# Performance work log

Measured on AMD Instinct MI355X. Metric: run time of the kernel, lower is better.

The kernel has to match this reference:

```python
import jax, jax.numpy as jnp
import numpy as np

# --- constants from loss_param_dict (fallback norm_info: means=0, stds=1 -> denorm is identity) ---
A_DIV, A_NS, A_BC = 0.3, 0.3, 0.3
A_LOSS = 1.0 - A_DIV - A_NS - A_BC
SCALE_BASE, SCALE_DIV, SCALE_NS, SCALE_BC = 300000.0, 1e-05, 0.01, 1.0
SX, SY = 1.2 / 127, 0.8 / 127  # spacing along axis 2 (x) and axis 1 (y)
RHO, MU = 1.0, 1.0
H, W = 128, 128
IN_TOP = H // 2 + H // 16 + 1  # 73
IN_BOT = H // 2 - H // 16 - 1  # 55
NORM_MEAN = np.array([0.0, 0.0, 0.0, 0.0], dtype=np.float32)
NORM_STD = np.array([1.0, 1.0, 1.0, 1.0], dtype=np.float32)


def grad_axis(f, h, axis):
    """torch.gradient: 2nd-order central interior, 1st-order one-sided edges."""
    f = jnp.moveaxis(f, axis, -1)
    left = (f[..., 1:2] - f[..., 0:1]) / h
    interior = (f[..., 2:] - f[..., :-2]) / (2.0 * h)
    right = (f[..., -1:] - f[..., -2:-1]) / h
    g = jnp.concatenate([left, interior, right], axis=-1)
    return jnp.moveaxis(g, -1, axis)


def setup_inputs() -> dict:
    key = jax.random.key(0)
    k1, k2, k3 = jax.random.split(key, 3)
    B = 256
    return {
        "inputs": jax.random.normal(k1, (B, 1, H, W), dtype=jnp.float32),
        "outputs": jax.random.normal(k2, (B, 3, H, W), dtype=jnp.float32),
        "targets": jax.random.normal(k3, (B, 3, H, W), dtype=jnp.float32),
    }


def reference(inputs, outputs, targets):
    # base MSE loss (reduction='sum')
    loss_base = jnp.sum((outputs - targets) ** 2) / SCALE_BASE

    # denormalisation (norm_info fallback: identity, but kept for faithfulness)
    in_ch = inputs.shape[1]
    mean = jnp.asarray(NORM_MEAN)
    std = jnp.asarray(NORM_STD)
    inp = inputs * std[:in_ch][None, :, None, None] + mean[:in_ch][None, :, None, None]
    out = outputs * std[in_ch:][None, :, None, None] + mean[in_ch:][None, :, None, None]

    # boundary residual pieces (on full, un-cropped denormalised outputs)
    pieces = [
        out[:, 1, IN_BOT:IN_TOP, 0].ravel() - 0.01,
        out[:, 0, IN_BOT:IN_TOP, -1].ravel(),
    ]
    for ch in (1, 2):
        for idx in (0, -1):
            pieces += [
                out[:, ch, idx, :].ravel(),
                out[:, ch, IN_TOP:, idx].ravel(),
                out[:, ch, 0:IN_BOT, idx].ravel(),
            ]
    boundary = jnp.concatenate(pieces)

    # interior crop [B, C, 126, 126]
    i_loc = inp[:, :, 1 : H - 1, 1 : W - 1]
    o_loc = out[:, :, 1 : H - 1, 1 : W - 1]

    p, u, v = o_loc[:, 0], o_loc[:, 1], o_loc[:, 2]  # [B,126,126]
    alpha = i_loc[:, 0]

    dp_dx, dp_dy = grad_axis(p, SX, 2), grad_axis(p, SY, 1)
    du_dx, du_dy = grad_axis(u, SX, 2), grad_axis(u, SY, 1)
    dv_dx, dv_dy = grad_axis(v, SX, 2), grad_axis(v, SY, 1)
    du_dxx = grad_axis(du_dx, SX, 2)
    du_dyy = grad_axis(du_dy, SY, 1)
    dv_dxx = grad_axis(dv_dx, SX, 2)
    dv_dyy = grad_axis(dv_dy, SY, 1)

    # continuity residual
    loss_cont = jnp.mean((du_dx + dv_dy) ** 2) / SCALE_DIV

    # Navier-Stokes residual
    x_res = u * du_dx + v * du_dy + dp_dx / RHO - MU * (du_dxx + du_dyy) / RHO + alpha * u / RHO
    y_res = u * dv_dx + v * dv_dy + dp_dy / RHO - MU * (dv_dxx + dv_dyy) / RHO + alpha * v / RHO
    mse_ns = (jnp.mean(x_res**2, axis=(1, 2)) + jnp.mean(y_res**2, axis=(1, 2))).mean() / 2.0
    loss_ns = mse_ns / SCALE_NS

    # boundary residual
    loss_bc = jnp.mean(boundary**2) / SCALE_BC

    return A_LOSS * loss_base + A_DIV * loss_cont + A_NS * loss_ns + A_BC * loss_bc
```

## Files before the change

### kernel.cpp

```cpp
#include <hip/hip_runtime.h>


#define HH 128
#define WW 128
#define NI 126
#define NBLK 4096

#define AS1C(p) ((const __attribute__((address_space(1))) void*)(p))
#define AS3(p)  ((__attribute__((address_space(3))) void*)(p))

template <int I> __device__ __forceinline__ float gc(const float4& f) {
    if constexpr (I == 0) return f.x;
    else if constexpr (I == 1) return f.y;
    else if constexpr (I == 2) return f.z;
    else return f.w;
}

template <int IDX>
__device__ __forceinline__ float xsel(const float4& l, const float4& m, const float4& r) {
    if constexpr (IDX < 4) return gc<IDX>(l);
    else if constexpr (IDX < 8) return gc<IDX - 4>(m);
    else return gc<IDX - 8>(r);
}

__device__ __forceinline__ float grad1s(float m1, float a0, float p1, int i,
                                        float inv_h, float inv_2h) {
    if (i == 0) return (p1 - a0) * inv_h;
    if (i == NI - 1) return (a0 - m1) * inv_h;
    return (p1 - m1) * inv_2h;
}

__device__ __forceinline__ float grad2s(float m2, float m1, float a0, float p1, float p2,
                                        int i, float inv_h, float inv_2h) {
    if (i == 0) {
        const float d1 = (p2 - a0) * inv_2h, d0 = (p1 - a0) * inv_h;
        return (d1 - d0) * inv_h;
    }
    if (i == 1) {
        const float d1 = (p2 - a0) * inv_2h, dm1 = (a0 - m1) * inv_h;
        return (d1 - dm1) * inv_2h;
    }
    if (i == NI - 1) {
        const float d0 = (a0 - m1) * inv_h, dm1 = (a0 - m2) * inv_2h;
        return (d0 - dm1) * inv_h;
    }
    if (i == NI - 2) {
        const float d1 = (p1 - a0) * inv_h, dm1 = (a0 - m2) * inv_2h;
        return (d1 - dm1) * inv_2h;
    }
    return (p2 - 2.f * a0 + m2) * inv_2h * inv_2h;
}

struct Acc { float base, bc, cont, ns; };

template <int Q>
__device__ __forceinline__ void do_pixel(
    int r, int c0, bool midrow,
    const float4& uxl, const float4& uxm, const float4& uxr,
    const float4& uym2, const float4& uym1, const float4& uyp1, const float4& uyp2,
    const float4& vxl, const float4& vxm, const float4& vxr,
    const float4& vym2, const float4& vym1, const float4& vyp1, const float4& vyp2,
    const float4& pxl, const float4& pxm, const float4& pxr,
    const float4& pym1, const float4& pyp1,
    const float4& t0, const float4& t1, const float4& t2, const float4& av,
    Acc& acc) {
    const int c = c0 + Q;
    const float u0 = xsel<Q + 4>(uxl, uxm, uxr);
    const float v0 = xsel<Q + 4>(vxl, vxm, vxr);
    const float p0 = xsel<Q + 4>(pxl, pxm, pxr);

    {
        const float d0 = p0 - gc<Q>(t0);
        const float d1 = u0 - gc<Q>(t1);
        const float d2 = v0 - gc<Q>(t2);
        acc.base += d0 * d0 + d1 * d1 + d2 * d2;
    }
    if (c == 0 && midrow) { const float d = u0 - 0.01f; acc.bc += d * d; }
    if (c == WW - 1 && midrow) { acc.bc += p0 * p0; }
    if (r == 0 || r == HH - 1) { acc.bc += u0 * u0 + v0 * v0; }
    if ((c == 0 || c == WW - 1) && !midrow) { acc.bc += u0 * u0 + v0 * v0; }

    if (r >= 1 && r <= HH - 2 && c >= 1 && c <= WW - 2) {
        const int ic = c - 1, ir = r - 1;
        const float inv_sx = 127.0f / 1.2f, inv_2sx = 127.0f / 2.4f;
        const float inv_sy = 127.0f / 0.8f, inv_2sy = 127.0f / 1.6f;

        const float uxm2 = xsel<Q + 2>(uxl, uxm, uxr), uxm1 = xsel<Q + 3>(uxl, uxm, uxr);
        const float uxp1 = xsel<Q + 5>(uxl, uxm, uxr), uxp2 = xsel<Q + 6>(uxl, uxm, uxr);
        const float vxm2 = xsel<Q + 2>(vxl, vxm, vxr), vxm1 = xsel<Q + 3>(vxl, vxm, vxr);
        const float vxp1 = xsel<Q + 5>(vxl, vxm, vxr), vxp2 = xsel<Q + 6>(vxl, vxm, vxr);
        const float pxm1 = xsel<Q + 3>(pxl, pxm, pxr), pxp1 = xsel<Q + 5>(pxl, pxm, pxr);
        const float uym2s = gc<Q>(uym2), uym1s = gc<Q>(uym1);
        const float uyp1s = gc<Q>(uyp1), uyp2s = gc<Q>(uyp2);
        const float vym2s = gc<Q>(vym2), vym1s = gc<Q>(vym1);
        const float vyp1s = gc<Q>(vyp1), vyp2s = gc<Q>(vyp2);
        const float pym1s = gc<Q>(pym1), pyp1s = gc<Q>(pyp1);

        const float du_dx = grad1s(uxm1, u0, uxp1, ic, inv_sx, inv_2sx);
        const float du_dy = grad1s(uym1s, u0, uyp1s, ir, inv_sy, inv_2sy);
        const float dv_dx = grad1s(vxm1, v0, vxp1, ic, inv_sx, inv_2sx);
        const float dv_dy = grad1s(vym1s, v0, vyp1s, ir, inv_sy, inv_2sy);
        const float dp_dx = grad1s(pxm1, p0, pxp1, ic, inv_sx, inv_2sx);
        const float dp_dy = grad1s(pym1s, p0, pyp1s, ir, inv_sy, inv_2sy);
        const float du_dxx = grad2s(uxm2, uxm1, u0, uxp1, uxp2, ic, inv_sx, inv_2sx);
        const float du_dyy = grad2s(uym2s, uym1s, u0, uyp1s, uyp2s, ir, inv_sy, inv_2sy);
        const float dv_dxx = grad2s(vxm2, vxm1, v0, vxp1, vxp2, ic, inv_sx, inv_2sx);
        const float dv_dyy = grad2s(vym2s, vym1s, v0, vyp1s, vyp2s, ir, inv_sy, inv_2sy);

        const float alpha = gc<Q>(av);
        const float dvg = du_dx + dv_dy;
        acc.cont += dvg * dvg;
        const float xr_ = u0 * du_dx + v0 * du_dy + dp_dx - (du_dxx + du_dyy) + alpha * u0;
        const float yr_ = u0 * dv_dx + v0 * dv_dy + dp_dy - (dv_dxx + dv_dyy) + alpha * v0;
        acc.ns += xr_ * xr_ + yr_ * yr_;
    }
}

__global__ __launch_bounds__(256) void physics_loss_kernel(
    const float* __restrict__ inp, const float* __restrict__ out,
    const float* __restrict__ tgt, double* __restrict__ ws) {
    const int tid = threadIdx.x;
    const int grp = tid & 31;
    const int rloc = tid >> 5;
    const int bid = ((blockIdx.x & 7) << 9) | (blockIdx.x >> 3);
    const int b = bid >> 4;
    const int r0 = (bid & 15) << 3;
    const int r = r0 | rloc;
    const int c0 = grp << 2;
    const int lane = tid & 63;
    const int wv = tid >> 6;

    const float* O = out + (size_t)b * 3 * HH * WW;
    const float* T = tgt + (size_t)b * 3 * HH * WW;
    const float* A = inp + (size_t)b * HH * WW;
    const float* P = O;
    const float* U = O + HH * WW;
    const float* V = O + 2 * HH * WW;

    __shared__ float tile[34][128];

    auto ld = [&](const float* base, int row, int gg) {
        return reinterpret_cast<const float4*>(base + row * WW)[gg];
    };
    const float4 t0 = ld(T, r, grp);
    const float4 t1 = ld(T + HH * WW, r, grp);
    const float4 t2 = ld(T + 2 * HH * WW, r, grp);
    const float4 av = ld(A, r, grp);

    const int lsub = lane >> 5;
    const int lcol = (lane & 31) << 2;
    for (int ci = wv; ci < 17; ci += 4) {
        const float* src;
        int grow;
        if (ci < 6)       { src = U; grow = r0 - 2 + ci * 2 + lsub; }
        else if (ci < 12) { src = V; grow = r0 - 2 + (ci - 6) * 2 + lsub; }
        else              { src = P; grow = r0 - 1 + (ci - 12) * 2 + lsub; }
        grow = grow < 0 ? 0 : (grow > 127 ? 127 : grow);
        const float* gaddr = src + grow * WW + lcol;
        __builtin_amdgcn_global_load_lds(AS1C(gaddr),
                                         AS3((char*)&tile[0][0] + ci * 1024),
                                         16, 0, 0);
    }
    __syncthreads();

    const int gl = grp == 0 ? 0 : grp - 1;
    const int gr = grp == 31 ? 31 : grp + 1;
    auto lrow = [&](int row) { return reinterpret_cast<const float4*>(&tile[row][0]); };
    const float4 uym2 = lrow(rloc)[grp],     uym1 = lrow(rloc + 1)[grp];
    const float4 uxl  = lrow(rloc + 2)[gl],  uxm  = lrow(rloc + 2)[grp];
    const float4 uxr  = lrow(rloc + 2)[gr];
    const float4 uyp1 = lrow(rloc + 3)[grp], uyp2 = lrow(rloc + 4)[grp];
    const float4 vym2 = lrow(12 + rloc)[grp],     vym1 = lrow(12 + rloc + 1)[grp];
    const float4 vxl  = lrow(12 + rloc + 2)[gl],  vxm  = lrow(12 + rloc + 2)[grp];
    const float4 vxr  = lrow(12 + rloc + 2)[gr];
    const float4 vyp1 = lrow(12 + rloc + 3)[grp], vyp2 = lrow(12 + rloc + 4)[grp];
    const float4 pym1 = lrow(24 + rloc)[grp];
    const float4 pxl  = lrow(24 + rloc + 1)[gl],  pxm  = lrow(24 + rloc + 1)[grp];
    const float4 pxr  = lrow(24 + rloc + 1)[gr];
    const float4 pyp1 = lrow(24 + rloc + 2)[grp];

    const bool midrow = (r >= 55 && r < 73);
    Acc acc = {0.f, 0.f, 0.f, 0.f};

    do_pixel<0>(r, c0, midrow, uxl, uxm, uxr, uym2, uym1, uyp1, uyp2,
                vxl, vxm, vxr, vym2, vym1, vyp1, vyp2,
                pxl, pxm, pxr, pym1, pyp1, t0, t1, t2, av, acc);
    do_pixel<1>(r, c0, midrow, uxl, uxm, uxr, uym2, uym1, uyp1, uyp2,
                vxl, vxm, vxr, vym2, vym1, vyp1, vyp2,
                pxl, pxm, pxr, pym1, pyp1, t0, t1, t2, av, acc);
    do_pixel<2>(r, c0, midrow, uxl, uxm, uxr, uym2, uym1, uyp1, uyp2,
                vxl, vxm, vxr, vym2, vym1, vyp1, vyp2,
                pxl, pxm, pxr, pym1, pyp1, t0, t1, t2, av, acc);
    do_pixel<3>(r, c0, midrow, uxl, uxm, uxr, uym2, uym1, uyp1, uyp2,
                vxl, vxm, vxr, vym2, vym1, vyp1, vyp2,
                pxl, pxm, pxr, pym1, pyp1, t0, t1, t2, av, acc);

    float a_base = acc.base, a_bc = acc.bc, a_cont = acc.cont, a_ns = acc.ns;
    #pragma unroll
    for (int off = 32; off > 0; off >>= 1) {
        a_base += __shfl_down(a_base, off);
        a_bc   += __shfl_down(a_bc, off);
        a_cont += __shfl_down(a_cont, off);
        a_ns   += __shfl_down(a_ns, off);
    }
    __shared__ float red[4][4];
    if (lane == 0) {
        red[wv][0] = a_base; red[wv][1] = a_bc;
        red[wv][2] = a_cont; red[wv][3] = a_ns;
    }
    __syncthreads();
    if (tid == 0) {
        double b0 = 0, b1 = 0, b2 = 0, b3 = 0;
        #pragma unroll
        for (int w = 0; w < 4; ++w) {
            b0 += red[w][0]; b1 += red[w][1]; b2 += red[w][2]; b3 += red[w][3];
        }
        double* slot = ws + (size_t)bid * 4;
        slot[0] = b0; slot[1] = b1; slot[2] = b2; slot[3] = b3;
    }
}

__global__ __launch_bounds__(256) void finalize_kernel(const double* __restrict__ ws,
                                                       float* __restrict__ out) {
    const int tid = threadIdx.x;
    double a0 = 0, a1 = 0, a2 = 0, a3 = 0;
    for (int b = tid; b < NBLK; b += 256) {
        const double* p = ws + (size_t)b * 4;
        a0 += p[0]; a1 += p[1]; a2 += p[2]; a3 += p[3];
    }
    #pragma unroll
    for (int off = 32; off > 0; off >>= 1) {
        a0 += __shfl_down(a0, off);
        a1 += __shfl_down(a1, off);
        a2 += __shfl_down(a2, off);
        a3 += __shfl_down(a3, off);
    }
    __shared__ double red[4][4];
    const int wave = tid >> 6, lane = tid & 63;
    if (lane == 0) {
        red[wave][0] = a0; red[wave][1] = a1; red[wave][2] = a2; red[wave][3] = a3;
    }
    __syncthreads();
    if (tid == 0) {
        double b0 = 0, b1 = 0, b2 = 0, b3 = 0;
        #pragma unroll
        for (int w = 0; w < 4; ++w) {
            b0 += red[w][0]; b1 += red[w][1]; b2 += red[w][2]; b3 += red[w][3];
        }
        const double loss_base = b0 / 300000.0;
        const double loss_cont = b2 / (256.0 * 126.0 * 126.0) / 1e-5;
        const double loss_ns   = b3 / (2.0 * 256.0 * 126.0 * 126.0) / 0.01;
        const double loss_bc   = b1 / (256.0 * 988.0);
        out[0] = (float)(0.10000000000000009 * loss_base +
                         0.3 * (loss_cont + loss_ns + loss_bc));
    }
}

extern "C" void kernel_launch(void* const* d_in, const int* in_sizes, int n_in,
                              void* d_out, int out_size, void* d_ws, size_t ws_size,
                              hipStream_t stream) {
    const float* inp = (const float*)d_in[0];
    const float* out = (const float*)d_in[1];
    const float* tgt = (const float*)d_in[2];
    float* o = (float*)d_out;
    double* ws = (double*)d_ws;

    hipLaunchKernelGGL(physics_loss_kernel, dim3(NBLK), dim3(256), 0, stream,
                       inp, out, tgt, ws);
    hipLaunchKernelGGL(finalize_kernel, dim3(1), dim3(256), 0, stream, ws, o);
}
```

Before: 37.75 us.

## Double-buffer LDS staging across four row tiles per block with async loads

Each block now processes four 8-row tiles (32 rows) instead of one, cutting the grid from 4096 to 1024 blocks. Loads for the next tile, now including targets and alpha, are issued into a second LDS buffer via global_load_lds while the current tile is computed, with hand-written vmcnt waits and barriers. The intent is to overlap memory latency with compute and amortize per-block overhead. The cost is a much larger LDS footprint (about 66KB per block), which limits occupancy, plus fragile hand-counted wait values.

```diff
diff --git a/kernel.cpp b/kernel.cpp
--- a/kernel.cpp
+++ b/kernel.cpp
@@ -4,7 +4,7 @@
 #define HH 128
 #define WW 128
 #define NI 126
-#define NBLK 4096
+#define NBLK 1024
 
 #define AS1C(p) ((const __attribute__((address_space(1))) void*)(p))
 #define AS3(p)  ((__attribute__((address_space(3))) void*)(p))
@@ -116,19 +116,18 @@
     }
 }
 
-__global__ __launch_bounds__(256) void physics_loss_kernel(
+__global__ __launch_bounds__(256, 2) void physics_loss_kernel(
     const float* __restrict__ inp, const float* __restrict__ out,
     const float* __restrict__ tgt, double* __restrict__ ws) {
     const int tid = threadIdx.x;
     const int grp = tid & 31;
     const int rloc = tid >> 5;
-    const int bid = ((blockIdx.x & 7) << 9) | (blockIdx.x >> 3);
-    const int b = bid >> 4;
-    const int r0 = (bid & 15) << 3;
-    const int r = r0 | rloc;
-    const int c0 = grp << 2;
     const int lane = tid & 63;
     const int wv = tid >> 6;
+    const int bid = ((blockIdx.x & 7) << 7) | (blockIdx.x >> 3);
+    const int b = bid >> 2;
+    const int tgrp = bid & 3;
+    const int c0 = grp << 2;
 
     const float* O = out + (size_t)b * 3 * HH * WW;
     const float* T = tgt + (size_t)b * 3 * HH * WW;
@@ -136,64 +135,97 @@
     const float* P = O;
     const float* U = O + HH * WW;
     const float* V = O + 2 * HH * WW;
-
-    __shared__ float tile[34][128];
-
-    auto ld = [&](const float* base, int row, int gg) {
-        return reinterpret_cast<const float4*>(base + row * WW)[gg];
-    };
-    const float4 t0 = ld(T, r, grp);
-    const float4 t1 = ld(T + HH * WW, r, grp);
-    const float4 t2 = ld(T + 2 * HH * WW, r, grp);
-    const float4 av = ld(A, r, grp);
+    const float* T0 = T;
+    const float* T1 = T + HH * WW;
+    const float* T2 = T + 2 * HH * WW;
+
+    __shared__ float stile[2][66][128];
+    __shared__ float red[4][4];
 
     const int lsub = lane >> 5;
     const int lcol = (lane & 31) << 2;
-    for (int ci = wv; ci < 17; ci += 4) {
-        const float* src;
-        int grow;
-        if (ci < 6)       { src = U; grow = r0 - 2 + ci * 2 + lsub; }
-        else if (ci < 12) { src = V; grow = r0 - 2 + (ci - 6) * 2 + lsub; }
-        else              { src = P; grow = r0 - 1 + (ci - 12) * 2 + lsub; }
-        grow = grow < 0 ? 0 : (grow > 127 ? 127 : grow);
-        const float* gaddr = src + grow * WW + lcol;
-        __builtin_amdgcn_global_load_lds(AS1C(gaddr),
-                                         AS3((char*)&tile[0][0] + ci * 1024),
-                                         16, 0, 0);
-    }
-    __syncthreads();
-
-    const int gl = grp == 0 ? 0 : grp - 1;
-    const int gr = grp == 31 ? 31 : grp + 1;
-    auto lrow = [&](int row) { return reinterpret_cast<const float4*>(&tile[row][0]); };
-    const float4 uym2 = lrow(rloc)[grp],     uym1 = lrow(rloc + 1)[grp];
-    const float4 uxl  = lrow(rloc + 2)[gl],  uxm  = lrow(rloc + 2)[grp];
-    const float4 uxr  = lrow(rloc + 2)[gr];
-    const float4 uyp1 = lrow(rloc + 3)[grp], uyp2 = lrow(rloc + 4)[grp];
-    const float4 vym2 = lrow(12 + rloc)[grp],     vym1 = lrow(12 + rloc + 1)[grp];
-    const float4 vxl  = lrow(12 + rloc + 2)[gl],  vxm  = lrow(12 + rloc + 2)[grp];
-    const float4 vxr  = lrow(12 + rloc + 2)[gr];
-    const float4 vyp1 = lrow(12 + rloc + 3)[grp], vyp2 = lrow(12 + rloc + 4)[grp];
-    const float4 pym1 = lrow(24 + rloc)[grp];
-    const float4 pxl  = lrow(24 + rloc + 1)[gl],  pxm  = lrow(24 + rloc + 1)[grp];
-    const float4 pxr  = lrow(24 + rloc + 1)[gr];
-    const float4 pyp1 = lrow(24 + rloc + 2)[grp];
-
-    const bool midrow = (r >= 55 && r < 73);
+
+    auto stage = [&](int bufIdx, int tt) {
+        const int r0s = (tgrp << 5) | (tt << 3);
+        #pragma unroll
+        for (int k = 0; k < 9; ++k) {
+            const int ci = wv + (k << 2);
+            if (ci < 33) {
+                const float* src;
+                int grow;
+                if (ci < 6)       { src = U; grow = r0s - 2 + 2 * ci + lsub; }
+                else if (ci < 12) { src = V; grow = r0s - 2 + 2 * (ci - 6) + lsub; }
+                else if (ci < 17) { src = P; grow = r0s - 1 + 2 * (ci - 12) + lsub; }
+                else {
+                    const int g2 = ci - 17;
+                    src = (g2 < 4) ? T0 : (g2 < 8) ? T1 : (g2 < 12) ? T2 : A;
+                    grow = r0s + ((g2 & 3) << 1) + lsub;
+                }
+                grow = grow < 0 ? 0 : (grow > 127 ? 127 : grow);
+                __builtin_amdgcn_global_load_lds(
+                    AS1C(src + grow * WW + lcol),
+                    AS3((char*)&stile[bufIdx][0][0] + ci * 1024), 16, 0, 0);
+            }
+        }
+    };
+
     Acc acc = {0.f, 0.f, 0.f, 0.f};
 
-    do_pixel<0>(r, c0, midrow, uxl, uxm, uxr, uym2, uym1, uyp1, uyp2,
-                vxl, vxm, vxr, vym2, vym1, vyp1, vyp2,
-                pxl, pxm, pxr, pym1, pyp1, t0, t1, t2, av, acc);
-    do_pixel<1>(r, c0, midrow, uxl, uxm, uxr, uym2, uym1, uyp1, uyp2,
-                vxl, vxm, vxr, vym2, vym1, vyp1, vyp2,
-                pxl, pxm, pxr, pym1, pyp1, t0, t1, t2, av, acc);
-    do_pixel<2>(r, c0, midrow, uxl, uxm, uxr, uym2, uym1, uyp1, uyp2,
-                vxl, vxm, vxr, vym2, vym1, vyp1, vyp2,
-                pxl, pxm, pxr, pym1, pyp1, t0, t1, t2, av, acc);
-    do_pixel<3>(r, c0, midrow, uxl, uxm, uxr, uym2, uym1, uyp1, uyp2,
-                vxl, vxm, vxr, vym2, vym1, vyp1, vyp2,
-                pxl, pxm, pxr, pym1, pyp1, t0, t1, t2, av, acc);
+    stage(0, 0);
+    #pragma unroll
+    for (int t = 0; t < 4; ++t) {
+        if (t < 3) stage((t + 1) & 1, t + 1);
+        __builtin_amdgcn_sched_barrier(0);
+        if (t < 3) {
+            if (wv == 0) asm volatile("s_waitcnt vmcnt(9)" ::: "memory");
+            else         asm volatile("s_waitcnt vmcnt(8)" ::: "memory");
+        } else {
+            asm volatile("s_waitcnt vmcnt(0)" ::: "memory");
+        }
+        __builtin_amdgcn_s_barrier();
+        __builtin_amdgcn_sched_barrier(0);
+
+        const int r0t = (tgrp << 5) | (t << 3);
+        const int r = r0t | rloc;
+        const float(*buf)[128] = stile[t & 1];
+        auto lrow = [&](int row) { return reinterpret_cast<const float4*>(&buf[row][0]); };
+        const int gl = grp == 0 ? 0 : grp - 1;
+        const int gr = grp == 31 ? 31 : grp + 1;
+        const float4 uym2 = lrow(rloc)[grp],     uym1 = lrow(rloc + 1)[grp];
+        const float4 uxl  = lrow(rloc + 2)[gl],  uxm  = lrow(rloc + 2)[grp];
+        const float4 uxr  = lrow(rloc + 2)[gr];
+        const float4 uyp1 = lrow(rloc + 3)[grp], uyp2 = lrow(rloc + 4)[grp];
+        const float4 vym2 = lrow(12 + rloc)[grp],     vym1 = lrow(12 + rloc + 1)[grp];
+        const float4 vxl  = lrow(12 + rloc + 2)[gl],  vxm  = lrow(12 + rloc + 2)[grp];
+        const float4 vxr  = lrow(12 + rloc + 2)[gr];
+        const float4 vyp1 = lrow(12 + rloc + 3)[grp], vyp2 = lrow(12 + rloc + 4)[grp];
+        const float4 pym1 = lrow(24 + rloc)[grp];
+        const float4 pxl  = lrow(24 + rloc + 1)[gl],  pxm  = lrow(24 + rloc + 1)[grp];
+        const float4 pxr  = lrow(24 + rloc + 1)[gr];
+        const float4 pyp1 = lrow(24 + rloc + 2)[grp];
+        const float4 t0 = lrow(34 + rloc)[grp];
+        const float4 t1 = lrow(42 + rloc)[grp];
+        const float4 t2 = lrow(50 + rloc)[grp];
+        const float4 av = lrow(58 + rloc)[grp];
+
+        const bool midrow = (r >= 55 && r < 73);
+        do_pixel<0>(r, c0, midrow, uxl, uxm, uxr, uym2, uym1, uyp1, uyp2,
+                    vxl, vxm, vxr, vym2, vym1, vyp1, vyp2,
+                    pxl, pxm, pxr, pym1, pyp1, t0, t1, t2, av, acc);
+        do_pixel<1>(r, c0, midrow, uxl, uxm, uxr, uym2, uym1, uyp1, uyp2,
+                    vxl, vxm, vxr, vym2, vym1, vyp1, vyp2,
+                    pxl, pxm, pxr, pym1, pyp1, t0, t1, t2, av, acc);
+        do_pixel<2>(r, c0, midrow, uxl, uxm, uxr, uym2, uym1, uyp1, uyp2,
+                    vxl, vxm, vxr, vym2, vym1, vyp1, vyp2,
+                    pxl, pxm, pxr, pym1, pyp1, t0, t1, t2, av, acc);
+        do_pixel<3>(r, c0, midrow, uxl, uxm, uxr, uym2, uym1, uyp1, uyp2,
+                    vxl, vxm, vxr, vym2, vym1, vyp1, vyp2,
+                    pxl, pxm, pxr, pym1, pyp1, t0, t1, t2, av, acc);
+
+        __builtin_amdgcn_sched_barrier(0);
+        __builtin_amdgcn_s_barrier();
+        __builtin_amdgcn_sched_barrier(0);
+    }
 
     float a_base = acc.base, a_bc = acc.bc, a_cont = acc.cont, a_ns = acc.ns;
     #pragma unroll
@@ -203,7 +235,6 @@
         a_cont += __shfl_down(a_cont, off);
         a_ns   += __shfl_down(a_ns, off);
     }
-    __shared__ float red[4][4];
     if (lane == 0) {
         red[wv][0] = a_base; red[wv][1] = a_bc;
         red[wv][2] = a_cont; red[wv][3] = a_ns;
```

Result: slower. 46.12 us (+22.2%).
